# Kernel optimization log

Hardware: AMD Instinct MI355X
Metric: run time of the kernel (lower is better)

The kernel has to match this reference:

```python
import jax, jax.numpy as jnp
import numpy as np


def setup_inputs() -> dict:
    key = jax.random.key(0)
    k1, k2, k3, k4 = jax.random.split(key, 4)
    B1, N1, B2, N2, D = 64, 128, 64, 128, 128
    v1 = jax.random.normal(k1, (B1, N1, D), dtype=jnp.float32)
    v2 = jax.random.normal(k2, (B2, N2, D), dtype=jnp.float32)
    sz1 = jax.random.randint(k3, (B1,), 0, 128, dtype=jnp.int64)
    sz2 = jax.random.randint(k4, (B2,), 0, 128, dtype=jnp.int64)
    return {"v1": v1, "sz1": sz1, "v2": v2, "sz2": sz2}


def reference(v1, sz1, v2, sz2):
    # v1: (B1, N1, D) padded node features; v2: (B2, N2, D)
    # Pairwise Euclidean distances dist[b1,b2,i,j] = ||v1[b1,i] - v2[b2,j]||
    # via the gemm identity instead of the original's 5D broadcast.
    x2 = jnp.sum(v1 * v1, axis=-1)                     # (B1, N1)
    y2 = jnp.sum(v2 * v2, axis=-1)                     # (B2, N2)
    xy = jnp.einsum('aid,bjd->abij', v1, v2)           # (B1, B2, N1, N2)
    sq = x2[:, None, :, None] + y2[None, :, None, :] - 2.0 * xy
    dist = jnp.sqrt(jnp.maximum(sq, 0.0))              # (B1, B2, N1, N2)

    N1, N2 = v1.shape[1], v2.shape[1]
    mask1 = jnp.arange(N1)[None, :] >= sz1[:, None]    # (B1, N1) padded v1 nodes
    mask2 = jnp.arange(N2)[None, :] >= sz2[:, None]    # (B2, N2) padded v2 nodes
    mask = mask1[:, None, :, None] | mask2[None, :, None, :]  # (B1, B2, N1, N2)

    # Original fills masked entries with the global max of the (unmasked) distances.
    maximum = dist.max()
    dm = jnp.where(mask, maximum, dist)

    bm1 = dm.min(axis=2)                               # min over v1 nodes -> (B1, B2, N2)
    bm2 = dm.min(axis=3)                               # min over v2 nodes -> (B1, B2, N1)
    bm1 = jnp.where(jnp.all(mask, axis=2), 0.0, bm1)   # zero fully-masked columns
    bm2 = jnp.where(jnp.all(mask, axis=3), 0.0, bm2)   # zero fully-masked rows

    return bm1.sum(axis=2) + bm2.sum(axis=2)           # (B1, B2)
```

## Files before the change

kernel.cpp:

```cpp
#include <hip/hip_runtime.h>
#include <math.h>


typedef __attribute__((ext_vector_type(8))) short short8;
typedef __attribute__((ext_vector_type(4))) float f32x4;
typedef unsigned int u32;
typedef unsigned short ushort_t;

static __device__ __forceinline__ ushort_t f32_to_bf16_rne(float f) {
    u32 b = __float_as_uint(f);
    b += 0x7FFFu + ((b >> 16) & 1u);
    return (ushort_t)(b >> 16);
}

#define DPPX1(x) __int_as_float(__builtin_amdgcn_update_dpp( \
    0, __float_as_int(x), 0xB1, 0xF, 0xF, true))
#define DPPX2(x) __int_as_float(__builtin_amdgcn_update_dpp( \
    0, __float_as_int(x), 0x4E, 0xF, 0xF, true))

__global__ __launch_bounds__(256) void softhd_pre(
    const float* __restrict__ v1, const float* __restrict__ v2,
    ushort_t* __restrict__ v1b, ushort_t* __restrict__ v2b,
    float* __restrict__ x2g, float* __restrict__ y2g)
{
    int flat = blockIdx.x * 256 + threadIdx.x;
    int c = flat & 15;
    int r = (flat >> 4) & 127;
    int b = (flat >> 11) & 63;
    int t = flat >> 17;

    const float* src = (t ? v2 : v1) + ((size_t)((b << 7) + r) << 7) + c * 8;
    char* dstp = (char*)((t ? v2b : v1b) + ((size_t)b << 14));

    float4 q0 = *(const float4*)(src);
    float4 q1 = *(const float4*)(src + 4);

    ushort_t h[8];
    h[0] = f32_to_bf16_rne(q0.x); h[1] = f32_to_bf16_rne(q0.y);
    h[2] = f32_to_bf16_rne(q0.z); h[3] = f32_to_bf16_rne(q0.w);
    h[4] = f32_to_bf16_rne(q1.x); h[5] = f32_to_bf16_rne(q1.y);
    h[6] = f32_to_bf16_rne(q1.z); h[7] = f32_to_bf16_rne(q1.w);

    float p = 0.f;
#pragma unroll
    for (int k = 0; k < 8; ++k) {
        float fv = __uint_as_float((u32)h[k] << 16);
        p += fv * fv;
    }

    uint4 w;
    w.x = (u32)h[0] | ((u32)h[1] << 16);
    w.y = (u32)h[2] | ((u32)h[3] << 16);
    w.z = (u32)h[4] | ((u32)h[5] << 16);
    w.w = (u32)h[6] | ((u32)h[7] << 16);

    int off = ((c >> 2) << 13) + ((r >> 3) << 9) + ((c & 3) << 7) + ((r & 7) << 4);
    *(uint4*)(dstp + off) = w;

    p += __shfl_xor(p, 1);
    p += __shfl_xor(p, 2);
    p += __shfl_xor(p, 4);
    p += __shfl_xor(p, 8);
    if (c == 0) (t ? y2g : x2g)[(b << 7) + r] = p;
}

__global__ __launch_bounds__(256, 3) void softhd_mfma(
    const ushort_t* __restrict__ v1b, const ushort_t* __restrict__ v2b,
    const float* __restrict__ x2g, const float* __restrict__ y2g,
    const int* __restrict__ sz1, const int* __restrict__ sz2,
    float* __restrict__ out)
{
    __shared__ __align__(16) ushort_t sA[4 * 4096];
    __shared__ __align__(16) ushort_t sB[2][4096];
    __shared__ float sx2[128], sy2[2][128];
    __shared__ u32 sbm1[2][128], sbm2[2][128];
    __shared__ float swsum[4];

    const int tid = threadIdx.x;
    const int lane = tid & 63;
    const int wid = tid >> 6;
    const int bid = ((blockIdx.x & 7) << 8) | (blockIdx.x >> 3);
    const int b1 = bid >> 5;
    const int b2base = (bid & 31) << 1;

    const char* gA = (const char*)(v1b + ((size_t)b1 << 14));
    const char* gB0 = (const char*)(v2b + ((size_t)(b2base + 0) << 14));
    const char* gB1 = (const char*)(v2b + ((size_t)(b2base + 1) << 14));

    const int n1 = min(max(sz1[b1], 0), 128);
    int n2v[2];
    n2v[0] = min(max(sz2[b2base + 0], 0), 128);
    n2v[1] = min(max(sz2[b2base + 1], 0), 128);

    if (tid < 128) {
        sx2[tid] = x2g[(b1 << 7) + tid];
    } else {
        sy2[0][tid - 128] = y2g[((b2base + 0) << 7) + (tid - 128)];
        sy2[1][tid - 128] = y2g[((b2base + 1) << 7) + (tid - 128)];
    }
    ((u32*)sbm1)[tid] = 0x7F800000u;
    ((u32*)sbm2)[tid] = 0x7F800000u;
    asm volatile("" ::: "memory");

#define STAGE_A()                                                            \
    {                                                                        \
        _Pragma("unroll")                                                    \
        for (int e = 0; e < 8; ++e) {                                        \
            int m16 = ((e << 8) + tid) << 4;                                 \
            __builtin_amdgcn_global_load_lds(                                \
                (const __attribute__((address_space(1))) u32*)(gA + m16),    \
                (__attribute__((address_space(3))) u32*)((char*)&sA[0] + m16),\
                16, 0, 0);                                                   \
        }                                                                    \
    }
#define STAGE_B(d, gB, q)                                                    \
    {                                                                        \
        _Pragma("unroll")                                                    \
        for (int e = 0; e < 2; ++e) {                                        \
            int m16 = ((e << 8) + tid) << 4;                                 \
            __builtin_amdgcn_global_load_lds(                                \
                (const __attribute__((address_space(1))) u32*)((gB) + ((q) << 13) + m16),\
                (__attribute__((address_space(3))) u32*)((char*)&sB[d][0] + m16),        \
                16, 0, 0);                                                   \
        }                                                                    \
    }
#define WAITV2()  asm volatile("s_waitcnt vmcnt(2)" ::: "memory")
#define WAITV0()  asm volatile("s_waitcnt vmcnt(0)" ::: "memory")
#define BAR()     asm volatile("s_barrier" ::: "memory")

    STAGE_A();
    STAGE_B(0, gB0, 0);
    STAGE_B(1, gB0, 1);

    const int qr = wid >> 1, qc = wid & 1;
    const int ibase = qr << 6, jbase = qc << 6;
    const int rf = lane & 15, kg = lane >> 4;
    const bool h0 = lane & 1, h1 = lane & 2, h2 = lane & 4, h3 = lane & 8;
    const bool h4 = lane & 16, h5 = lane & 32;

    int aoff[4], boff[4];
#pragma unroll
    for (int f = 0; f < 4; ++f) {
        int ra = ibase + (f << 4) + rf;
        int rb = jbase + (f << 4) + rf;
        aoff[f] = ((ra >> 3) << 8) + (kg << 6) + ((ra & 7) << 3);
        boff[f] = ((rb >> 3) << 8) + (kg << 6) + ((rb & 7) << 3);
    }

    f32x4 acc[4][4];
#pragma unroll
    for (int fi = 0; fi < 4; ++fi)
#pragma unroll
        for (int fj = 0; fj < 4; ++fj)
            acc[fi][fj] = (f32x4){0.f, 0.f, 0.f, 0.f};

#define COMPUTE(d, q)                                                        \
    {                                                                        \
        short8 a[4], b[4];                                                   \
        _Pragma("unroll")                                                    \
        for (int f = 0; f < 4; ++f) {                                        \
            a[f] = *(const short8*)(&sA[(q) << 12] + aoff[f]);               \
            b[f] = *(const short8*)(&sB[d][0] + boff[f]);                    \
        }                                                                    \
        __builtin_amdgcn_s_setprio(1);                                       \
        _Pragma("unroll")                                                    \
        for (int fi = 0; fi < 4; ++fi)                                       \
            _Pragma("unroll")                                                \
            for (int fj = 0; fj < 4; ++fj)                                   \
                acc[fi][fj] = __builtin_amdgcn_mfma_f32_16x16x32_bf16(       \
                    a[fi], b[fj], acc[fi][fj], 0, 0, 0);                     \
        __builtin_amdgcn_s_setprio(0);                                       \
    }

    const float INF = __builtin_inff();

#define EPILOGUE(p)                                                          \
    {                                                                        \
        const int nn2 = n2v[p];                                              \
        float yje[4];                                                        \
        _Pragma("unroll")                                                    \
        for (int fj = 0; fj < 4; ++fj) {                                     \
            int j = jbase + (fj << 4) + rf;                                  \
            yje[fj] = (j < nn2) ? sy2[p][j] : INF;                           \
        }                                                                    \
        float minj[4] = {INF, INF, INF, INF};                                \
        float mini4[4];                                                      \
        _Pragma("unroll")                                                    \
        for (int fi = 0; fi < 4; ++fi) {                                     \
            const int i0 = ibase + (fi << 4) + (kg << 2);                    \
            float4 xs = *(const float4*)&sx2[i0];                            \
            float xie[4];                                                    \
            xie[0] = (i0 + 0 < n1) ? xs.x : INF;                             \
            xie[1] = (i0 + 1 < n1) ? xs.y : INF;                             \
            xie[2] = (i0 + 2 < n1) ? xs.z : INF;                             \
            xie[3] = (i0 + 3 < n1) ? xs.w : INF;                             \
            float u[4][4];                                                   \
            _Pragma("unroll")                                                \
            for (int fj = 0; fj < 4; ++fj) {                                 \
                _Pragma("unroll")                                            \
                for (int q = 0; q < 4; ++q)                                  \
                    u[fj][q] = fmaf(acc[fi][fj][q], -2.f, xie[q] + yje[fj]); \
                minj[fj] = fminf(fminf(minj[fj], u[fj][0]), u[fj][1]);       \
                minj[fj] = fminf(fminf(minj[fj], u[fj][2]), u[fj][3]);       \
            }                                                                \
            float mq0 = fminf(fminf(u[0][0], u[1][0]), fminf(u[2][0], u[3][0])); \
            float mq1 = fminf(fminf(u[0][1], u[1][1]), fminf(u[2][1], u[3][1])); \
            float mq2 = fminf(fminf(u[0][2], u[1][2]), fminf(u[2][2], u[3][2])); \
            float mq3 = fminf(fminf(u[0][3], u[1][3]), fminf(u[2][3], u[3][3])); \
            float pa = fminf(mq0, DPPX1(mq0));                               \
            float pb = fminf(mq1, DPPX1(mq1));                               \
            float r01 = h0 ? pb : pa;                                        \
            pa = fminf(mq2, DPPX1(mq2));                                     \
            pb = fminf(mq3, DPPX1(mq3));                                     \
            float r23 = h0 ? pb : pa;                                        \
            pa = fminf(r01, DPPX2(r01));                                     \
            pb = fminf(r23, DPPX2(r23));                                     \
            mini4[fi] = h1 ? pb : pa;                                        \
        }                                                                    \
        {                                                                    \
            float pa = fminf(mini4[0], __shfl_xor(mini4[0], 4));             \
            float pb = fminf(mini4[1], __shfl_xor(mini4[1], 4));             \
            float A = h2 ? pb : pa;                                          \
            pa = fminf(mini4[2], __shfl_xor(mini4[2], 4));                   \
            pb = fminf(mini4[3], __shfl_xor(mini4[3], 4));                   \
            float B = h2 ? pb : pa;                                          \
            pa = fminf(A, __shfl_xor(A, 8));                                 \
            pb = fminf(B, __shfl_xor(B, 8));                                 \
            float Mi = h3 ? pb : pa;                                         \
            float dmin = __builtin_amdgcn_sqrtf(fmaxf(Mi, 0.f));             \
            int ii = ibase + ((rf >> 2) << 4) + (kg << 2) + (rf & 3);        \
            atomicMin(&sbm2[p][ii], __float_as_uint(dmin));                  \
        }                                                                    \
        {                                                                    \
            float pa = fminf(minj[0], __shfl_xor(minj[0], 32));              \
            float pb = fminf(minj[1], __shfl_xor(minj[1], 32));              \
            float A = h5 ? pb : pa;                                          \
            pa = fminf(minj[2], __shfl_xor(minj[2], 32));                    \
            pb = fminf(minj[3], __shfl_xor(minj[3], 32));                    \
            float B = h5 ? pb : pa;                                          \
            pa = fminf(A, __shfl_xor(A, 16));                                \
            pb = fminf(B, __shfl_xor(B, 16));                                \
            float Mj = h4 ? pb : pa;                                         \
            float dminj = __builtin_amdgcn_sqrtf(fmaxf(Mj, 0.f));            \
            int fjf = ((lane >> 5) & 1) | (((lane >> 4) & 1) << 1);          \
            atomicMin(&sbm1[p][jbase + (fjf << 4) + rf], __float_as_uint(dminj)); \
        }                                                                    \
    }

    WAITV2(); BAR(); COMPUTE(0, 0); BAR(); STAGE_B(0, gB0, 2);
    WAITV2(); BAR(); COMPUTE(1, 1); BAR(); STAGE_B(1, gB0, 3);
    WAITV2(); BAR(); COMPUTE(0, 2); BAR(); STAGE_B(0, gB1, 0);
    WAITV2(); BAR(); COMPUTE(1, 3); BAR(); STAGE_B(1, gB1, 1);
    EPILOGUE(0);

#pragma unroll
    for (int fi = 0; fi < 4; ++fi)
#pragma unroll
        for (int fj = 0; fj < 4; ++fj)
            acc[fi][fj] = (f32x4){0.f, 0.f, 0.f, 0.f};

    WAITV2(); BAR(); COMPUTE(0, 0); BAR(); STAGE_B(0, gB1, 2);
    WAITV2(); BAR(); COMPUTE(1, 1); BAR(); STAGE_B(1, gB1, 3);
    WAITV2(); BAR(); COMPUTE(0, 2); BAR();
    WAITV0(); BAR(); COMPUTE(1, 3);
    EPILOGUE(1);

#undef COMPUTE
#undef STAGE_A
#undef STAGE_B
#undef EPILOGUE
#undef WAITV2
#undef WAITV0
#undef BAR

    __syncthreads();

    {
        const int p = tid >> 7;
        const int e = tid & 127;
        const int nn2 = n2v[p];
        float v = 0.f;
        if (n1 > 0 && e < nn2) v += __uint_as_float(sbm1[p][e]);
        if (nn2 > 0 && e < n1) v += __uint_as_float(sbm2[p][e]);
#pragma unroll
        for (int off = 32; off >= 1; off >>= 1) v += __shfl_down(v, off);
        if (lane == 0) swsum[wid] = v;
    }
    __syncthreads();
    if (tid == 0)   out[(b1 << 6) + b2base + 0] = swsum[0] + swsum[1];
    if (tid == 128) out[(b1 << 6) + b2base + 1] = swsum[2] + swsum[3];
}

extern "C" void kernel_launch(void* const* d_in, const int* in_sizes, int n_in,
                              void* d_out, int out_size, void* d_ws, size_t ws_size,
                              hipStream_t stream) {
    const float* v1  = (const float*)d_in[0];
    const int*   sz1 = (const int*)d_in[1];
    const float* v2  = (const float*)d_in[2];
    const int*   sz2 = (const int*)d_in[3];
    float* out = (float*)d_out;
    (void)in_sizes; (void)n_in; (void)out_size; (void)ws_size;

    char* ws = (char*)d_ws;
    ushort_t* v1b = (ushort_t*)ws;
    ushort_t* v2b = (ushort_t*)(ws + (2u << 20));
    float*    x2g = (float*)(ws + (4u << 20));
    float*    y2g = x2g + 64 * 128;

    softhd_pre<<<dim3(1024), dim3(256), 0, stream>>>(v1, v2, v1b, v2b, x2g, y2g);
    softhd_mfma<<<dim3(2048), dim3(256), 0, stream>>>(v1b, v2b, x2g, y2g,
                                                      sz1, sz2, out);
}
```

Baseline: 33.90 us.

## Load B fragments directly from global into registers, dropping LDS staging

The B operand (v2 bf16 tiles) is no longer staged through shared memory with global_load_lds. Each wave now reads its MFMA B fragments straight from global memory into registers, double-buffered one K-chunk ahead. This removes the sB buffer and the per-stage waitcnt/barrier pairs, leaving a single __syncthreads after the A tile loads. In exchange, the two waves that share a column half both fetch the same B data, and global load latency is hidden only by a one-stage register prefetch, so some of it may stay exposed.

Measured after the change: 31.79 us. -6.2%, faster.

```diff
diff --git a/kernel.cpp b/kernel.cpp
--- a/kernel.cpp
+++ b/kernel.cpp
@@ -71,7 +71,6 @@
     float* __restrict__ out)
 {
     __shared__ __align__(16) ushort_t sA[4 * 4096];
-    __shared__ __align__(16) ushort_t sB[2][4096];
     __shared__ float sx2[128], sy2[2][128];
     __shared__ u32 sbm1[2][128], sbm2[2][128];
     __shared__ float swsum[4];
@@ -92,6 +91,15 @@
     n2v[0] = min(max(sz2[b2base + 0], 0), 128);
     n2v[1] = min(max(sz2[b2base + 1], 0), 128);
 
+#pragma unroll
+    for (int e = 0; e < 8; ++e) {
+        int m16 = ((e << 8) + tid) << 4;
+        __builtin_amdgcn_global_load_lds(
+            (const __attribute__((address_space(1))) u32*)(gA + m16),
+            (__attribute__((address_space(3))) u32*)((char*)&sA[0] + m16),
+            16, 0, 0);
+    }
+
     if (tid < 128) {
         sx2[tid] = x2g[(b1 << 7) + tid];
     } else {
@@ -100,37 +108,7 @@
     }
     ((u32*)sbm1)[tid] = 0x7F800000u;
     ((u32*)sbm2)[tid] = 0x7F800000u;
-    asm volatile("" ::: "memory");
-
-#define STAGE_A()                                                            \
-    {                                                                        \
-        _Pragma("unroll")                                                    \
-        for (int e = 0; e < 8; ++e) {                                        \
-            int m16 = ((e << 8) + tid) << 4;                                 \
-            __builtin_amdgcn_global_load_lds(                                \
-                (const __attribute__((address_space(1))) u32*)(gA + m16),    \
-                (__attribute__((address_space(3))) u32*)((char*)&sA[0] + m16),\
-                16, 0, 0);                                                   \
-        }                                                                    \
-    }
-#define STAGE_B(d, gB, q)                                                    \
-    {                                                                        \
-        _Pragma("unroll")                                                    \
-        for (int e = 0; e < 2; ++e) {                                        \
-            int m16 = ((e << 8) + tid) << 4;                                 \
-            __builtin_amdgcn_global_load_lds(                                \
-                (const __attribute__((address_space(1))) u32*)((gB) + ((q) << 13) + m16),\
-                (__attribute__((address_space(3))) u32*)((char*)&sB[d][0] + m16),        \
-                16, 0, 0);                                                   \
-        }                                                                    \
-    }
-#define WAITV2()  asm volatile("s_waitcnt vmcnt(2)" ::: "memory")
-#define WAITV0()  asm volatile("s_waitcnt vmcnt(0)" ::: "memory")
-#define BAR()     asm volatile("s_barrier" ::: "memory")
-
-    STAGE_A();
-    STAGE_B(0, gB0, 0);
-    STAGE_B(1, gB0, 1);
+    __syncthreads();
 
     const int qr = wid >> 1, qc = wid & 1;
     const int ibase = qr << 6, jbase = qc << 6;
@@ -138,13 +116,13 @@
     const bool h0 = lane & 1, h1 = lane & 2, h2 = lane & 4, h3 = lane & 8;
     const bool h4 = lane & 16, h5 = lane & 32;
 
-    int aoff[4], boff[4];
+    int aoff[4], boffB[4];
 #pragma unroll
     for (int f = 0; f < 4; ++f) {
         int ra = ibase + (f << 4) + rf;
         int rb = jbase + (f << 4) + rf;
-        aoff[f] = ((ra >> 3) << 8) + (kg << 6) + ((ra & 7) << 3);
-        boff[f] = ((rb >> 3) << 8) + (kg << 6) + ((rb & 7) << 3);
+        aoff[f]  = ((ra >> 3) << 8) + (kg << 6) + ((ra & 7) << 3);
+        boffB[f] = ((rb >> 3) << 9) + (kg << 7) + ((rb & 7) << 4);
     }
 
     f32x4 acc[4][4];
@@ -154,21 +132,25 @@
         for (int fj = 0; fj < 4; ++fj)
             acc[fi][fj] = (f32x4){0.f, 0.f, 0.f, 0.f};
 
-#define COMPUTE(d, q)                                                        \
+#define LOADB(B, gB, q)                                                      \
     {                                                                        \
-        short8 a[4], b[4];                                                   \
-        _Pragma("unroll")                                                    \
-        for (int f = 0; f < 4; ++f) {                                        \
+        _Pragma("unroll")                                                    \
+        for (int f = 0; f < 4; ++f)                                          \
+            B[f] = *(const short8*)((gB) + ((q) << 13) + boffB[f]);          \
+    }
+#define COMP(B, q)                                                           \
+    {                                                                        \
+        short8 a[4];                                                         \
+        _Pragma("unroll")                                                    \
+        for (int f = 0; f < 4; ++f)                                          \
             a[f] = *(const short8*)(&sA[(q) << 12] + aoff[f]);               \
-            b[f] = *(const short8*)(&sB[d][0] + boff[f]);                    \
-        }                                                                    \
         __builtin_amdgcn_s_setprio(1);                                       \
         _Pragma("unroll")                                                    \
         for (int fi = 0; fi < 4; ++fi)                                       \
             _Pragma("unroll")                                                \
             for (int fj = 0; fj < 4; ++fj)                                   \
                 acc[fi][fj] = __builtin_amdgcn_mfma_f32_16x16x32_bf16(       \
-                    a[fi], b[fj], acc[fi][fj], 0, 0, 0);                     \
+                    a[fi], B[fj], acc[fi][fj], 0, 0, 0);                     \
         __builtin_amdgcn_s_setprio(0);                                       \
     }
 
@@ -247,10 +229,14 @@
         }                                                                    \
     }
 
-    WAITV2(); BAR(); COMPUTE(0, 0); BAR(); STAGE_B(0, gB0, 2);
-    WAITV2(); BAR(); COMPUTE(1, 1); BAR(); STAGE_B(1, gB0, 3);
-    WAITV2(); BAR(); COMPUTE(0, 2); BAR(); STAGE_B(0, gB1, 0);
-    WAITV2(); BAR(); COMPUTE(1, 3); BAR(); STAGE_B(1, gB1, 1);
+    short8 bfA[4], bfB[4];
+
+    LOADB(bfA, gB0, 0); LOADB(bfB, gB0, 1);
+    COMP(bfA, 0); LOADB(bfA, gB0, 2);
+    COMP(bfB, 1); LOADB(bfB, gB0, 3);
+    COMP(bfA, 2);
+    COMP(bfB, 3);
+    LOADB(bfA, gB1, 0); LOADB(bfB, gB1, 1);
     EPILOGUE(0);
 
 #pragma unroll
@@ -259,19 +245,15 @@
         for (int fj = 0; fj < 4; ++fj)
             acc[fi][fj] = (f32x4){0.f, 0.f, 0.f, 0.f};
 
-    WAITV2(); BAR(); COMPUTE(0, 0); BAR(); STAGE_B(0, gB1, 2);
-    WAITV2(); BAR(); COMPUTE(1, 1); BAR(); STAGE_B(1, gB1, 3);
-    WAITV2(); BAR(); COMPUTE(0, 2); BAR();
-    WAITV0(); BAR(); COMPUTE(1, 3);
+    COMP(bfA, 0); LOADB(bfA, gB1, 2);
+    COMP(bfB, 1); LOADB(bfB, gB1, 3);
+    COMP(bfA, 2);
+    COMP(bfB, 3);
     EPILOGUE(1);
 
-#undef COMPUTE
-#undef STAGE_A
-#undef STAGE_B
+#undef LOADB
+#undef COMP
 #undef EPILOGUE
-#undef WAITV2
-#undef WAITV0
-#undef BAR
 
     __syncthreads();
 
```
